# Performance work log

Measured on AMD Instinct MI355X. Metric: run time of the kernel, lower is better.

The kernel has to match this reference:

```python
import jax, jax.numpy as jnp
import numpy as np

N = 100000   # nodes
E = 1600000  # edges
G = 64       # graphs in batch
D = 128      # input_dim
H = 128      # hidden dim (both layers)
C = 10       # output classes
EPS = 1e-5


def setup_inputs() -> dict:
    key = jax.random.key(0)
    ks = jax.random.split(key, 8)
    x = jax.random.normal(ks[0], (N, D), dtype=jnp.float32)
    edge_index = jax.random.randint(ks[1], (2, E), 0, N, dtype=jnp.int32)
    batch = jnp.sort(jax.random.randint(ks[2], (N,), 0, G, dtype=jnp.int32))
    s1 = 1.0 / np.sqrt(D)
    s2 = 1.0 / np.sqrt(H)
    return {
        "x": x, "edge_index": edge_index, "batch": batch,
        "W1": jax.random.uniform(ks[3], (D, H), jnp.float32, -s1, s1),
        "b1": jnp.zeros((H,), jnp.float32),
        "gw1": jnp.ones((H,), jnp.float32),   # GraphNorm weight
        "gb1": jnp.zeros((H,), jnp.float32),  # GraphNorm bias
        "ga1": jnp.ones((H,), jnp.float32),   # GraphNorm mean_scale
        "W2": jax.random.uniform(ks[4], (H, H), jnp.float32, -s2, s2),
        "b2": jnp.zeros((H,), jnp.float32),
        "gw2": jnp.ones((H,), jnp.float32),
        "gb2": jnp.zeros((H,), jnp.float32),
        "ga2": jnp.ones((H,), jnp.float32),
        "Wc": jax.random.uniform(ks[5], (H, C), jnp.float32, -s2, s2),
        "bc": jnp.zeros((C,), jnp.float32),
    }


def _gcn_conv(x, W, b, row, col, deg_inv_sqrt):
    # PyG GCNConv: h = D^-1/2 (A+I) D^-1/2 (x W) + b  (self-loops already in row/col)
    h = x @ W                                   # [N, H]
    norm = deg_inv_sqrt[row] * deg_inv_sqrt[col]  # [E+N]
    msgs = h[row] * norm[:, None]               # gather + scale  [E+N, H]
    out = jax.ops.segment_sum(msgs, col, num_segments=N)  # scatter-add
    return out + b


def _graph_norm(x, batch, counts, weight, bias, mean_scale):
    # PyG GraphNorm: (x - alpha*mean_g) / sqrt(var_g + eps) * weight + bias
    mean = jax.ops.segment_sum(x, batch, num_segments=G) / counts  # [G, H]
    sub = x - mean_scale * mean[batch]
    var = jax.ops.segment_sum(sub * sub, batch, num_segments=G) / counts
    return weight * sub / jnp.sqrt(var[batch] + EPS) + bias


def reference(x, edge_index, batch, W1, b1, gw1, gb1, ga1,
              W2, b2, gw2, gb2, ga2, Wc, bc):
    loops = jnp.arange(N, dtype=edge_index.dtype)
    row = jnp.concatenate([edge_index[0], loops])  # source
    col = jnp.concatenate([edge_index[1], loops])  # target
    deg = jax.ops.segment_sum(jnp.ones_like(col, dtype=x.dtype), col, num_segments=N)
    dis = jnp.where(deg > 0, jax.lax.rsqrt(deg), 0.0)
    counts = jnp.maximum(
        jax.ops.segment_sum(jnp.ones((N,), x.dtype), batch, num_segments=G), 1.0
    )[:, None]  # nodes per graph [G, 1]

    h = jax.nn.relu(_gcn_conv(x, W1, b1, row, col, dis))
    h = _graph_norm(h, batch, counts, gw1, gb1, ga1)
    h = jax.nn.relu(_gcn_conv(h, W2, b2, row, col, dis))
    h = _graph_norm(h, batch, counts, gw2, gb2, ga2)
    # global_mean_pool over graphs, classifier, softmax
    pooled = jax.ops.segment_sum(h, batch, num_segments=G) / counts  # [G, H]
    logits = pooled @ Wc + bc
    return jax.nn.softmax(logits, axis=1)
```

## Files before the change

### kernel.cpp

```cpp
#include <hip/hip_runtime.h>
#include <cstdint>

#define NN 100000
#define NE 1600000
#define NG 64
#define NH 128
#define NC 10
#define EPSV 1e-5f

#define NB 782
#define NBLK 512
#define EPB ((NE + NBLK - 1) / NBLK)
#define NSCAN (NB * NBLK)
#define NSB (NSCAN / 1024)

typedef __attribute__((ext_vector_type(8))) short bf16x8;
typedef __attribute__((ext_vector_type(4))) float f32x4;
typedef __attribute__((ext_vector_type(2))) float f32x2;
typedef unsigned long long u64;
typedef unsigned char uchar;

__device__ __forceinline__ ushort f2b(float f) {
  uint u = __builtin_bit_cast(uint, f);
  u = (u + 0x7FFFu + ((u >> 16) & 1u)) >> 16;
  return (ushort)u;
}
__device__ __forceinline__ float b2f(ushort h) {
  return __builtin_bit_cast(float, ((uint)h) << 16);
}

__global__ __launch_bounds__(256) void k_prep0(const int* __restrict__ batch,
                                               int* __restrict__ gstart, int* __restrict__ counts,
                                               u64* __restrict__ zrowA, u64* __restrict__ zrowB,
                                               const float* __restrict__ W1, ushort* __restrict__ WF1,
                                               const float* __restrict__ W2, ushort* __restrict__ WF2,
                                               const int* __restrict__ ei, int* __restrict__ ghist) {
  int b = blockIdx.x;
  if (b == 0) {
    __shared__ int lb[NG + 1];
    int t = threadIdx.x;
    if (t <= NG) {
      int lo = 0, hi = NN;
      while (lo < hi) { int mid = (lo + hi) >> 1; if (batch[mid] < t) lo = mid + 1; else hi = mid; }
      lb[t] = lo;
    }
    if (t >= 96 && t < 112) zrowA[t - 96] = 0ull;
    if (t >= 112 && t < 128) zrowB[t - 112] = 0ull;
    __syncthreads();
    if (t < NG) { gstart[t] = lb[t]; counts[t] = lb[t + 1] - lb[t]; }
    if (t == 0) gstart[NG] = NN;
  } else if (b <= 16) {
    int tt = (b - 1) * 256 + threadIdx.x;
    const float* W = (tt < 2048) ? W1 : W2;
    ushort* WF = (tt < 2048) ? WF1 : WF2;
    int t = tt & 2047;
    int lane = t & 63, nk = t >> 6;
    int n = nk >> 2, ks = nk & 3;
    int col = n * 16 + (lane & 15);
    int k0 = ks * 32 + (lane >> 4) * 8;
#pragma unroll
    for (int j = 0; j < 8; ++j) WF[(size_t)t * 8 + j] = f2b(W[(k0 + j) * NH + col]);
  } else {
    __shared__ int h[NB];
    int t = threadIdx.x, blk = b - 17;
    for (int i = t; i < NB; i += 256) h[i] = 0;
    __syncthreads();
    int e0 = blk * EPB, e1 = min(NE, e0 + EPB);
    for (int e = e0 + t; e < e1; e += 256) atomicAdd(&h[ei[NE + e] >> 7], 1);
    __syncthreads();
    for (int i = t; i < NB; i += 256) ghist[i * NBLK + blk] = h[i];
  }
}

__global__ __launch_bounds__(256) void k_scan1g(int* __restrict__ data, int* __restrict__ bsums) {
  __shared__ int sh[256];
  int t = threadIdx.x;
  int base = blockIdx.x * 1024 + t * 4;
  int4 v = *reinterpret_cast<const int4*>(data + base);
  int s = v.x + v.y + v.z + v.w;
  sh[t] = s;
  __syncthreads();
  for (int o = 1; o < 256; o <<= 1) {
    int x = (t >= o) ? sh[t - o] : 0;
    __syncthreads();
    sh[t] += x;
    __syncthreads();
  }
  int ex = sh[t] - s;
  int4 o4;
  o4.x = ex; o4.y = ex + v.x; o4.z = ex + v.x + v.y; o4.w = ex + v.x + v.y + v.z;
  *reinterpret_cast<int4*>(data + base) = o4;
  if (t == 255) bsums[blockIdx.x] = sh[255];
}

__global__ __launch_bounds__(512) void k_scan2(int* bsums, int nb) {
  __shared__ int sh[512];
  int t = threadIdx.x;
  int v = (t < nb) ? bsums[t] : 0;
  sh[t] = v;
  __syncthreads();
  for (int o = 1; o < 512; o <<= 1) {
    int x = (t >= o) ? sh[t - o] : 0;
    __syncthreads();
    sh[t] += x;
    __syncthreads();
  }
  if (t < nb) bsums[t] = sh[t] - v;
}

__global__ __launch_bounds__(256) void k_scan3g(int* __restrict__ data, const int* __restrict__ bsums) {
  int t = threadIdx.x;
  int base = blockIdx.x * 1024 + t * 4;
  int add = bsums[blockIdx.x];
  int4 v = *reinterpret_cast<int4*>(data + base);
  v.x += add; v.y += add; v.z += add; v.w += add;
  *reinterpret_cast<int4*>(data + base) = v;
}

__global__ __launch_bounds__(256) void k_scatter(const int* __restrict__ ei, const int* __restrict__ ghist,
                                                 int* __restrict__ tmp) {
  __shared__ int cur[NB];
  int t = threadIdx.x, blk = blockIdx.x;
  for (int i = t; i < NB; i += 256) cur[i] = ghist[i * NBLK + blk];
  __syncthreads();
  int e0 = blk * EPB, e1 = min(NE, e0 + EPB);
  for (int e = e0 + t; e < e1; e += 256) {
    int d = ei[NE + e], s = ei[e];
    int p = atomicAdd(&cur[d >> 7], 1);
    tmp[p] = ((d & 127) << 17) | s;
  }
}

__global__ __launch_bounds__(256) void k_fine(const int* __restrict__ tmp, const int* __restrict__ ghist,
                                              int* __restrict__ deg, int* __restrict__ offs,
                                              float* __restrict__ dis, int* __restrict__ csr) {
  __shared__ int fh[128], fsc[128], fc[128];
  int b = blockIdx.x, t = threadIdx.x;
  int bs = ghist[b * NBLK];
  int be = (b + 1 < NB) ? ghist[(b + 1) * NBLK] : NE;
  if (t < 128) fh[t] = 0;
  __syncthreads();
  for (int e = bs + t; e < be; e += 256) atomicAdd(&fh[tmp[e] >> 17], 1);
  __syncthreads();
  if (t < 128) fsc[t] = fh[t];
  __syncthreads();
  for (int o = 1; o < 128; o <<= 1) {
    int x = 0;
    if (t < 128 && t >= o) x = fsc[t - o];
    __syncthreads();
    if (t < 128) fsc[t] += x;
    __syncthreads();
  }
  if (t < 128) {
    int ex = fsc[t] - fh[t];
    int node = b * 128 + t;
    fc[t] = bs + ex;
    if (node < NN) {
      deg[node] = fh[t];
      offs[node] = bs + ex;
      dis[node] = rsqrtf((float)(fh[t] + 1));
    }
  }
  __syncthreads();
  for (int e = bs + t; e < be; e += 256) {
    int v = tmp[e];
    int p = atomicAdd(&fc[v >> 17], 1);
    csr[p] = v & 0x1FFFF;
  }
}

template <bool NORM>
__global__ __launch_bounds__(256) void k_gemm(const void* __restrict__ Xv, const ushort* __restrict__ WF,
                                              const float* __restrict__ dis, const int* __restrict__ batch,
                                              const float* __restrict__ Aaff, const float* __restrict__ Baff,
                                              uchar* __restrict__ out) {
  __shared__ uint sds[4][512];
  int t = threadIdx.x;
  int w = t >> 6, lane = t & 63;
  int r0 = blockIdx.x * 64 + w * 16;
  int arow = r0 + (lane & 15);
  int khi = lane >> 4;
  int arowc = (arow < NN) ? arow : (NN - 1);

  f32x4 acc[8];
#pragma unroll
  for (int n = 0; n < 8; ++n) acc[n] = (f32x4){0.f, 0.f, 0.f, 0.f};

  int g = 0;
  if (NORM) g = batch[arowc];
  const bf16x8* WFv = reinterpret_cast<const bf16x8*>(WF);

#pragma unroll
  for (int ks = 0; ks < 4; ++ks) {
    int k0 = ks * 32 + khi * 8;
    bf16x8 a;
    if (!NORM) {
      const float* X = (const float*)Xv;
      float4 x0 = *reinterpret_cast<const float4*>(X + (size_t)arowc * NH + k0);
      float4 x1 = *reinterpret_cast<const float4*>(X + (size_t)arowc * NH + k0 + 4);
      a[0] = (short)f2b(x0.x); a[1] = (short)f2b(x0.y); a[2] = (short)f2b(x0.z); a[3] = (short)f2b(x0.w);
      a[4] = (short)f2b(x1.x); a[5] = (short)f2b(x1.y); a[6] = (short)f2b(x1.z); a[7] = (short)f2b(x1.w);
    } else {
      const uchar* X8 = (const uchar*)Xv;
      u64 v = *reinterpret_cast<const u64*>(X8 + (size_t)arowc * NH + k0);
      uint lo = (uint)v, hi = (uint)(v >> 32);
      f32x2 x01 = __builtin_amdgcn_cvt_pk_f32_fp8((int)lo, false);
      f32x2 x23 = __builtin_amdgcn_cvt_pk_f32_fp8((int)lo, true);
      f32x2 x45 = __builtin_amdgcn_cvt_pk_f32_fp8((int)hi, false);
      f32x2 x67 = __builtin_amdgcn_cvt_pk_f32_fp8((int)hi, true);
      float4 A0 = *reinterpret_cast<const float4*>(Aaff + g * NH + k0);
      float4 A1 = *reinterpret_cast<const float4*>(Aaff + g * NH + k0 + 4);
      float4 B0 = *reinterpret_cast<const float4*>(Baff + g * NH + k0);
      float4 B1 = *reinterpret_cast<const float4*>(Baff + g * NH + k0 + 4);
      a[0] = (short)f2b(fmaf(A0.x, x01[0], B0.x));
      a[1] = (short)f2b(fmaf(A0.y, x01[1], B0.y));
      a[2] = (short)f2b(fmaf(A0.z, x23[0], B0.z));
      a[3] = (short)f2b(fmaf(A0.w, x23[1], B0.w));
      a[4] = (short)f2b(fmaf(A1.x, x45[0], B1.x));
      a[5] = (short)f2b(fmaf(A1.y, x45[1], B1.y));
      a[6] = (short)f2b(fmaf(A1.z, x67[0], B1.z));
      a[7] = (short)f2b(fmaf(A1.w, x67[1], B1.w));
    }
#pragma unroll
    for (int n = 0; n < 8; ++n) {
      bf16x8 b = WFv[(n * 4 + ks) * 64 + lane];
      acc[n] = __builtin_amdgcn_mfma_f32_16x16x32_bf16(a, b, acc[n], 0, 0, 0);
    }
  }

  int colb = lane & 15;
  uchar* sb = (uchar*)sds[w];
#pragma unroll
  for (int reg = 0; reg < 4; ++reg) {
    int row = khi * 4 + reg;
    int grow = r0 + row;
    float d = (grow < NN) ? dis[grow] : 0.f;
#pragma unroll
    for (int n = 0; n < 8; n += 2) {
      int p2 = __builtin_amdgcn_cvt_pk_fp8_f32(acc[n][reg] * d, acc[n + 1][reg] * d, 0, false);
      sb[row * 128 + n * 16 + colb] = (uchar)(p2 & 0xFF);
      sb[row * 128 + (n + 1) * 16 + colb] = (uchar)((p2 >> 8) & 0xFF);
    }
  }
  __syncthreads();
  const u64* ss = (const u64*)sds[w];
  u64* gout = (u64*)(out + (size_t)r0 * 128);
#pragma unroll
  for (int it = 0; it < 4; ++it) {
    int idx = it * 64 + lane;
    int row = idx >> 4;
    if (r0 + row < NN) __builtin_nontemporal_store(ss[idx], &gout[idx]);
  }
}

__global__ __launch_bounds__(256) void k_agg(const u64* __restrict__ hf8, const int* __restrict__ offs,
                                             const int* __restrict__ deg, const int* __restrict__ csr,
                                             const float* __restrict__ dis, const float* __restrict__ bias,
                                             u64* __restrict__ outb) {
  int w = threadIdx.x >> 6, lane = threadIdx.x & 63;
  int grp = lane >> 4, sub = lane & 15;
  int node = blockIdx.x * 4 + w;
  if (node >= NN) return;
  f32x2 a01 = (f32x2){0.f, 0.f}, a23 = (f32x2){0.f, 0.f};
  f32x2 a45 = (f32x2){0.f, 0.f}, a67 = (f32x2){0.f, 0.f};
#define ACCUM(V)                                                          \
  {                                                                       \
    uint lo_ = (uint)(V), hi_ = (uint)((V) >> 32);                        \
    a01 += __builtin_amdgcn_cvt_pk_f32_fp8((int)lo_, false);              \
    a23 += __builtin_amdgcn_cvt_pk_f32_fp8((int)lo_, true);               \
    a45 += __builtin_amdgcn_cvt_pk_f32_fp8((int)hi_, false);              \
    a67 += __builtin_amdgcn_cvt_pk_f32_fp8((int)hi_, true);               \
  }
#define BATCH(IBASE)                                                      \
  {                                                                       \
    int p0 = beg + (IBASE) + grp;                                         \
    int c0 = __builtin_nontemporal_load(csr + min(p0, lim));              \
    int c1 = __builtin_nontemporal_load(csr + min(p0 + 4, lim));          \
    int c2 = __builtin_nontemporal_load(csr + min(p0 + 8, lim));          \
    int c3 = __builtin_nontemporal_load(csr + min(p0 + 12, lim));         \
    int s0 = (p0 <= lim) ? c0 : NN;                                       \
    int s1 = (p0 + 4 <= lim) ? c1 : NN;                                   \
    int s2 = (p0 + 8 <= lim) ? c2 : NN;                                   \
    int s3 = (p0 + 12 <= lim) ? c3 : NN;                                  \
    u64 v0 = hf8[(size_t)s0 * 16 + sub];                                  \
    u64 v1 = hf8[(size_t)s1 * 16 + sub];                                  \
    u64 v2 = hf8[(size_t)s2 * 16 + sub];                                  \
    u64 v3 = hf8[(size_t)s3 * 16 + sub];                                  \
    ACCUM(v0); ACCUM(v1); ACCUM(v2); ACCUM(v3);                           \
  }
  int beg = __builtin_nontemporal_load(offs + node);
  int cnt = __builtin_nontemporal_load(deg + node);
  if (grp == 0) {
    u64 v = hf8[(size_t)node * 16 + sub];
    ACCUM(v);
  }
  int lim = beg + cnt - 1;
  BATCH(0);
  if (cnt > 16) {
    BATCH(16);
    for (int i = 32; i < cnt; i += 16) BATCH(i);
  }
#undef BATCH
#undef ACCUM
  float a0 = a01[0], a1 = a01[1], a2 = a23[0], a3 = a23[1];
  float a4 = a45[0], a5 = a45[1], a6 = a67[0], a7 = a67[1];
  a0 += __shfl_xor(a0, 16); a0 += __shfl_xor(a0, 32);
  a1 += __shfl_xor(a1, 16); a1 += __shfl_xor(a1, 32);
  a2 += __shfl_xor(a2, 16); a2 += __shfl_xor(a2, 32);
  a3 += __shfl_xor(a3, 16); a3 += __shfl_xor(a3, 32);
  a4 += __shfl_xor(a4, 16); a4 += __shfl_xor(a4, 32);
  a5 += __shfl_xor(a5, 16); a5 += __shfl_xor(a5, 32);
  a6 += __shfl_xor(a6, 16); a6 += __shfl_xor(a6, 32);
  a7 += __shfl_xor(a7, 16); a7 += __shfl_xor(a7, 32);
  if (grp == 0) {
    float d = dis[node];
    float4 bA = *reinterpret_cast<const float4*>(bias + sub * 8);
    float4 bB = *reinterpret_cast<const float4*>(bias + sub * 8 + 4);
    float o0 = fmaxf(fmaf(d, a0, bA.x), 0.f);
    float o1 = fmaxf(fmaf(d, a1, bA.y), 0.f);
    float o2 = fmaxf(fmaf(d, a2, bA.z), 0.f);
    float o3 = fmaxf(fmaf(d, a3, bA.w), 0.f);
    float o4 = fmaxf(fmaf(d, a4, bB.x), 0.f);
    float o5 = fmaxf(fmaf(d, a5, bB.y), 0.f);
    float o6 = fmaxf(fmaf(d, a6, bB.z), 0.f);
    float o7 = fmaxf(fmaf(d, a7, bB.w), 0.f);
    uint b01 = (uint)__builtin_amdgcn_cvt_pk_fp8_f32(o0, o1, 0, false) & 0xFFFFu;
    uint b23 = (uint)__builtin_amdgcn_cvt_pk_fp8_f32(o2, o3, 0, false) & 0xFFFFu;
    uint b45 = (uint)__builtin_amdgcn_cvt_pk_fp8_f32(o4, o5, 0, false) & 0xFFFFu;
    uint b67 = (uint)__builtin_amdgcn_cvt_pk_fp8_f32(o6, o7, 0, false) & 0xFFFFu;
    u64 pk = (u64)(b01 | (b23 << 16)) | ((u64)(b45 | (b67 << 16)) << 32);
    __builtin_nontemporal_store(pk, &outb[(size_t)node * 16 + sub]);
  }
}

__global__ __launch_bounds__(256) void k_stats(const uint* __restrict__ t8, const int* __restrict__ gstart,
                                               float* __restrict__ acc) {
  int g = blockIdx.x >> 4, s = blockIdx.x & 15;
  int beg = gstart[g], end = gstart[g + 1];
  int j = threadIdx.x & 31, q = threadIdx.x >> 5;
  f32x2 s01 = (f32x2){0.f, 0.f}, s23 = (f32x2){0.f, 0.f};
  f32x2 q01 = (f32x2){0.f, 0.f}, q23 = (f32x2){0.f, 0.f};
  for (int n = beg + s * 8 + q; n < end; n += 128) {
    uint v = t8[(size_t)n * 32 + j];
    f32x2 f01 = __builtin_amdgcn_cvt_pk_f32_fp8((int)v, false);
    f32x2 f23 = __builtin_amdgcn_cvt_pk_f32_fp8((int)v, true);
    s01 += f01; s23 += f23;
    q01 += f01 * f01; q23 += f23 * f23;
  }
  __shared__ float shs[256][4];
  __shared__ float shq[256][4];
  int t = threadIdx.x;
  shs[t][0] = s01[0]; shs[t][1] = s01[1]; shs[t][2] = s23[0]; shs[t][3] = s23[1];
  shq[t][0] = q01[0]; shq[t][1] = q01[1]; shq[t][2] = q23[0]; shq[t][3] = q23[1];
  __syncthreads();
  if (q == 0) {
    float sm[4], sq[4];
#pragma unroll
    for (int k = 0; k < 4; ++k) { sm[k] = shs[j][k]; sq[k] = shq[j][k]; }
#pragma unroll
    for (int qq = 1; qq < 8; ++qq) {
      int idx = qq * 32 + j;
#pragma unroll
      for (int k = 0; k < 4; ++k) { sm[k] += shs[idx][k]; sq[k] += shq[idx][k]; }
    }
    int f = j * 4;
    float* dst = acc + (size_t)(s * NG + g) * 2 * NH;
#pragma unroll
    for (int k = 0; k < 4; ++k) { dst[f + k] = sm[k]; dst[NH + f + k] = sq[k]; }
  }
}

__global__ __launch_bounds__(128) void k_fin1(const float* __restrict__ acc, const int* __restrict__ counts,
                                              const float* __restrict__ gw, const float* __restrict__ gb,
                                              const float* __restrict__ ga,
                                              float* __restrict__ Aaff, float* __restrict__ Baff) {
  int g = blockIdx.x, f = threadIdx.x;
  float sum = 0.f, sq = 0.f;
#pragma unroll 4
  for (int s = 0; s < 16; ++s) {
    const float* d = acc + (size_t)(s * NG + g) * 2 * NH;
    sum += d[f];
    sq += d[NH + f];
  }
  float cnt = fmaxf((float)counts[g], 1.f);
  float m = sum / cnt;
  float ex2 = sq / cnt;
  float a = ga[f];
  float var = ex2 - 2.f * a * m * m + a * a * m * m;
  float rstd = rsqrtf(var + EPSV);
  float A = gw[f] * rstd;
  Aaff[g * NH + f] = A;
  Baff[g * NH + f] = gb[f] - A * a * m;
}

__global__ __launch_bounds__(128) void k_fin2head(const float* __restrict__ acc, const int* __restrict__ counts,
                                                  const float* __restrict__ gw, const float* __restrict__ gb,
                                                  const float* __restrict__ ga, const float* __restrict__ Wc,
                                                  const float* __restrict__ bc, float* __restrict__ outp) {
  __shared__ float pool[NH];
  __shared__ float lg[NC];
  int g = blockIdx.x, f = threadIdx.x;
  float sum = 0.f, sq = 0.f;
#pragma unroll 4
  for (int s = 0; s < 16; ++s) {
    const float* d = acc + (size_t)(s * NG + g) * 2 * NH;
    sum += d[f];
    sq += d[NH + f];
  }
  float cnt = fmaxf((float)counts[g], 1.f);
  float m = sum / cnt;
  float ex2 = sq / cnt;
  float a = ga[f];
  float var = ex2 - 2.f * a * m * m + a * a * m * m;
  float rstd = rsqrtf(var + EPSV);
  pool[f] = gw[f] * rstd * (m - a * m) + gb[f];
  __syncthreads();
  if (f < NC) {
    float s = bc[f];
    for (int h = 0; h < NH; ++h) s = fmaf(pool[h], Wc[h * NC + f], s);
    lg[f] = s;
  }
  __syncthreads();
  if (f == 0) {
    float mx = lg[0];
    for (int c = 1; c < NC; ++c) mx = fmaxf(mx, lg[c]);
    float ex[NC];
    float ssum = 0.f;
    for (int c = 0; c < NC; ++c) { ex[c] = __expf(lg[c] - mx); ssum += ex[c]; }
    float inv = 1.f / ssum;
    for (int c = 0; c < NC; ++c) outp[g * NC + c] = ex[c] * inv;
  }
}

extern "C" void kernel_launch(void* const* d_in, const int* in_sizes, int n_in,
                              void* d_out, int out_size, void* d_ws, size_t ws_size,
                              hipStream_t stream) {
  const float* x   = (const float*)d_in[0];
  const int*   ei  = (const int*)d_in[1];
  const int*   bat = (const int*)d_in[2];
  const float* W1  = (const float*)d_in[3];
  const float* b1  = (const float*)d_in[4];
  const float* gw1 = (const float*)d_in[5];
  const float* gb1 = (const float*)d_in[6];
  const float* ga1 = (const float*)d_in[7];
  const float* W2  = (const float*)d_in[8];
  const float* b2  = (const float*)d_in[9];
  const float* gw2 = (const float*)d_in[10];
  const float* gb2 = (const float*)d_in[11];
  const float* ga2 = (const float*)d_in[12];
  const float* Wc  = (const float*)d_in[13];
  const float* bc  = (const float*)d_in[14];
  float* outp = (float*)d_out;

  char* ws = (char*)d_ws;
  size_t off = 0;
  auto alloc = [&](size_t b) { size_t p = off; off += (b + 255) & ~(size_t)255; return p; };
  int*    deg     = (int*)(ws + alloc((size_t)NN * 4));
  float*  dis     = (float*)(ws + alloc((size_t)NN * 4));
  int*    counts  = (int*)(ws + alloc(NG * 4));
  int*    gstart  = (int*)(ws + alloc((NG + 1) * 4));
  int*    offs    = (int*)(ws + alloc((size_t)NN * 4));
  int*    bsums   = (int*)(ws + alloc(512 * 4));
  int*    csr     = (int*)(ws + alloc((size_t)NE * 4));
  float*  statacc = (float*)(ws + alloc((size_t)16 * NG * 2 * NH * 4));
  float*  Aaff    = (float*)(ws + alloc((size_t)NG * NH * 4));
  float*  Baff    = (float*)(ws + alloc((size_t)NG * NH * 4));
  ushort* WF1     = (ushort*)(ws + alloc((size_t)2048 * 8 * 2));
  ushort* WF2     = (ushort*)(ws + alloc((size_t)2048 * 8 * 2));
  uchar*  bufA    = (uchar*)(ws + alloc((size_t)(NN + 1) * NH));
  uchar*  bufB    = (uchar*)(ws + alloc((size_t)(NN + 1) * NH));
  int* tmp   = (int*)bufB;
  int* ghist = (int*)((char*)bufB + (((size_t)NE * 4 + 255) & ~(size_t)255));
  (void)ws_size; (void)in_sizes; (void)n_in; (void)out_size;

  u64* zrowA = (u64*)(bufA + (size_t)NN * NH);
  u64* zrowB = (u64*)(bufB + (size_t)NN * NH);

  k_prep0<<<529, 256, 0, stream>>>(bat, gstart, counts, zrowA, zrowB, W1, WF1, W2, WF2, ei, ghist);
  k_scan1g<<<NSB, 256, 0, stream>>>(ghist, bsums);
  k_scan2<<<1, 512, 0, stream>>>(bsums, NSB);
  k_scan3g<<<NSB, 256, 0, stream>>>(ghist, bsums);
  k_scatter<<<NBLK, 256, 0, stream>>>(ei, ghist, tmp);
  k_fine<<<NB, 256, 0, stream>>>(tmp, ghist, deg, offs, dis, csr);

  int gemm_grid = (NN + 63) / 64;
  int agg_grid  = (NN + 3) / 4;

  k_gemm<false><<<gemm_grid, 256, 0, stream>>>(x, WF1, dis, bat, nullptr, nullptr, bufA);
  k_agg<<<agg_grid, 256, 0, stream>>>((const u64*)bufA, offs, deg, csr, dis, b1, (u64*)bufB);
  k_stats<<<NG * 16, 256, 0, stream>>>((const uint*)bufB, gstart, statacc);
  k_fin1<<<NG, 128, 0, stream>>>(statacc, counts, gw1, gb1, ga1, Aaff, Baff);

  k_gemm<true><<<gemm_grid, 256, 0, stream>>>(bufB, WF2, dis, bat, Aaff, Baff, bufA);
  k_agg<<<agg_grid, 256, 0, stream>>>((const u64*)bufA, offs, deg, csr, dis, b2, (u64*)bufB);
  k_stats<<<NG * 16, 256, 0, stream>>>((const uint*)bufB, gstart, statacc);
  k_fin2head<<<NG, 128, 0, stream>>>(statacc, counts, gw2, gb2, ga2, Wc, bc, outp);
}
```

Measured before the change: 221.9 us.

## Map one 16-lane group per node in aggregation and fold scan fixup into consumers

The aggregation kernel now assigns each 16-lane group its own destination node instead of having four groups share one node. Each group walks its full neighbour list in batches of 16 loads, which removes the cross-group shuffle reduction and lets all four groups write output. Separately, the scan add-back kernel is dropped, and the scatter and fine-binning kernels add the block prefix sums on the fly. The aggregation change raises register use for 16 outstanding loads per lane, and it can cause divergence when nodes in one wave have different degrees. It also relies on NN being divisible by 16, since the bounds check was removed.

```diff
diff --git a/kernel.cpp b/kernel.cpp
--- a/kernel.cpp
+++ b/kernel.cpp
@@ -108,20 +108,14 @@
   if (t < nb) bsums[t] = sh[t] - v;
 }
 
-__global__ __launch_bounds__(256) void k_scan3g(int* __restrict__ data, const int* __restrict__ bsums) {
-  int t = threadIdx.x;
-  int base = blockIdx.x * 1024 + t * 4;
-  int add = bsums[blockIdx.x];
-  int4 v = *reinterpret_cast<int4*>(data + base);
-  v.x += add; v.y += add; v.z += add; v.w += add;
-  *reinterpret_cast<int4*>(data + base) = v;
-}
-
 __global__ __launch_bounds__(256) void k_scatter(const int* __restrict__ ei, const int* __restrict__ ghist,
-                                                 int* __restrict__ tmp) {
+                                                 const int* __restrict__ bsums, int* __restrict__ tmp) {
   __shared__ int cur[NB];
   int t = threadIdx.x, blk = blockIdx.x;
-  for (int i = t; i < NB; i += 256) cur[i] = ghist[i * NBLK + blk];
+  for (int i = t; i < NB; i += 256) {
+    int idx = i * NBLK + blk;
+    cur[i] = ghist[idx] + bsums[idx >> 10];
+  }
   __syncthreads();
   int e0 = blk * EPB, e1 = min(NE, e0 + EPB);
   for (int e = e0 + t; e < e1; e += 256) {
@@ -132,12 +126,18 @@
 }
 
 __global__ __launch_bounds__(256) void k_fine(const int* __restrict__ tmp, const int* __restrict__ ghist,
+                                              const int* __restrict__ bsums,
                                               int* __restrict__ deg, int* __restrict__ offs,
                                               float* __restrict__ dis, int* __restrict__ csr) {
   __shared__ int fh[128], fsc[128], fc[128];
   int b = blockIdx.x, t = threadIdx.x;
-  int bs = ghist[b * NBLK];
-  int be = (b + 1 < NB) ? ghist[(b + 1) * NBLK] : NE;
+  int idx0 = b * NBLK;
+  int bs = ghist[idx0] + bsums[idx0 >> 10];
+  int be = NE;
+  if (b + 1 < NB) {
+    int idx1 = (b + 1) * NBLK;
+    be = ghist[idx1] + bsums[idx1 >> 10];
+  }
   if (t < 128) fh[t] = 0;
   __syncthreads();
   for (int e = bs + t; e < be; e += 256) atomicAdd(&fh[tmp[e] >> 17], 1);
@@ -259,8 +259,7 @@
                                              u64* __restrict__ outb) {
   int w = threadIdx.x >> 6, lane = threadIdx.x & 63;
   int grp = lane >> 4, sub = lane & 15;
-  int node = blockIdx.x * 4 + w;
-  if (node >= NN) return;
+  int node = (blockIdx.x * 4 + w) * 4 + grp;
   f32x2 a01 = (f32x2){0.f, 0.f}, a23 = (f32x2){0.f, 0.f};
   f32x2 a45 = (f32x2){0.f, 0.f}, a67 = (f32x2){0.f, 0.f};
 #define ACCUM(V)                                                          \
@@ -271,66 +270,51 @@
     a45 += __builtin_amdgcn_cvt_pk_f32_fp8((int)hi_, false);              \
     a67 += __builtin_amdgcn_cvt_pk_f32_fp8((int)hi_, true);               \
   }
+  int beg = __builtin_nontemporal_load(offs + node);
+  int cnt = __builtin_nontemporal_load(deg + node);
+  {
+    u64 v = hf8[(size_t)node * 16 + sub];
+    ACCUM(v);
+  }
+  int lim = max(beg + cnt - 1, 0);
+  int endp = beg + cnt;
 #define BATCH(IBASE)                                                      \
   {                                                                       \
-    int p0 = beg + (IBASE) + grp;                                         \
-    int c0 = __builtin_nontemporal_load(csr + min(p0, lim));              \
-    int c1 = __builtin_nontemporal_load(csr + min(p0 + 4, lim));          \
-    int c2 = __builtin_nontemporal_load(csr + min(p0 + 8, lim));          \
-    int c3 = __builtin_nontemporal_load(csr + min(p0 + 12, lim));         \
-    int s0 = (p0 <= lim) ? c0 : NN;                                       \
-    int s1 = (p0 + 4 <= lim) ? c1 : NN;                                   \
-    int s2 = (p0 + 8 <= lim) ? c2 : NN;                                   \
-    int s3 = (p0 + 12 <= lim) ? c3 : NN;                                  \
-    u64 v0 = hf8[(size_t)s0 * 16 + sub];                                  \
-    u64 v1 = hf8[(size_t)s1 * 16 + sub];                                  \
-    u64 v2 = hf8[(size_t)s2 * 16 + sub];                                  \
-    u64 v3 = hf8[(size_t)s3 * 16 + sub];                                  \
-    ACCUM(v0); ACCUM(v1); ACCUM(v2); ACCUM(v3);                           \
-  }
-  int beg = __builtin_nontemporal_load(offs + node);
-  int cnt = __builtin_nontemporal_load(deg + node);
-  if (grp == 0) {
-    u64 v = hf8[(size_t)node * 16 + sub];
-    ACCUM(v);
-  }
-  int lim = beg + cnt - 1;
+    int pb = beg + (IBASE);                                               \
+    int c_[16];                                                           \
+    _Pragma("unroll")                                                     \
+    for (int j = 0; j < 16; ++j)                                          \
+      c_[j] = __builtin_nontemporal_load(csr + min(pb + j, lim));         \
+    u64 v_[16];                                                           \
+    _Pragma("unroll")                                                     \
+    for (int j = 0; j < 16; ++j) {                                        \
+      int s = (pb + j < endp) ? c_[j] : NN;                               \
+      v_[j] = hf8[(size_t)s * 16 + sub];                                  \
+    }                                                                     \
+    _Pragma("unroll")                                                     \
+    for (int j = 0; j < 16; ++j) ACCUM(v_[j]);                            \
+  }
   BATCH(0);
-  if (cnt > 16) {
-    BATCH(16);
-    for (int i = 32; i < cnt; i += 16) BATCH(i);
-  }
+  for (int i = 16; i < cnt; i += 16) BATCH(i);
 #undef BATCH
 #undef ACCUM
-  float a0 = a01[0], a1 = a01[1], a2 = a23[0], a3 = a23[1];
-  float a4 = a45[0], a5 = a45[1], a6 = a67[0], a7 = a67[1];
-  a0 += __shfl_xor(a0, 16); a0 += __shfl_xor(a0, 32);
-  a1 += __shfl_xor(a1, 16); a1 += __shfl_xor(a1, 32);
-  a2 += __shfl_xor(a2, 16); a2 += __shfl_xor(a2, 32);
-  a3 += __shfl_xor(a3, 16); a3 += __shfl_xor(a3, 32);
-  a4 += __shfl_xor(a4, 16); a4 += __shfl_xor(a4, 32);
-  a5 += __shfl_xor(a5, 16); a5 += __shfl_xor(a5, 32);
-  a6 += __shfl_xor(a6, 16); a6 += __shfl_xor(a6, 32);
-  a7 += __shfl_xor(a7, 16); a7 += __shfl_xor(a7, 32);
-  if (grp == 0) {
-    float d = dis[node];
-    float4 bA = *reinterpret_cast<const float4*>(bias + sub * 8);
-    float4 bB = *reinterpret_cast<const float4*>(bias + sub * 8 + 4);
-    float o0 = fmaxf(fmaf(d, a0, bA.x), 0.f);
-    float o1 = fmaxf(fmaf(d, a1, bA.y), 0.f);
-    float o2 = fmaxf(fmaf(d, a2, bA.z), 0.f);
-    float o3 = fmaxf(fmaf(d, a3, bA.w), 0.f);
-    float o4 = fmaxf(fmaf(d, a4, bB.x), 0.f);
-    float o5 = fmaxf(fmaf(d, a5, bB.y), 0.f);
-    float o6 = fmaxf(fmaf(d, a6, bB.z), 0.f);
-    float o7 = fmaxf(fmaf(d, a7, bB.w), 0.f);
-    uint b01 = (uint)__builtin_amdgcn_cvt_pk_fp8_f32(o0, o1, 0, false) & 0xFFFFu;
-    uint b23 = (uint)__builtin_amdgcn_cvt_pk_fp8_f32(o2, o3, 0, false) & 0xFFFFu;
-    uint b45 = (uint)__builtin_amdgcn_cvt_pk_fp8_f32(o4, o5, 0, false) & 0xFFFFu;
-    uint b67 = (uint)__builtin_amdgcn_cvt_pk_fp8_f32(o6, o7, 0, false) & 0xFFFFu;
-    u64 pk = (u64)(b01 | (b23 << 16)) | ((u64)(b45 | (b67 << 16)) << 32);
-    __builtin_nontemporal_store(pk, &outb[(size_t)node * 16 + sub]);
-  }
+  float d = dis[node];
+  float4 bA = *reinterpret_cast<const float4*>(bias + sub * 8);
+  float4 bB = *reinterpret_cast<const float4*>(bias + sub * 8 + 4);
+  float o0 = fmaxf(fmaf(d, a01[0], bA.x), 0.f);
+  float o1 = fmaxf(fmaf(d, a01[1], bA.y), 0.f);
+  float o2 = fmaxf(fmaf(d, a23[0], bA.z), 0.f);
+  float o3 = fmaxf(fmaf(d, a23[1], bA.w), 0.f);
+  float o4 = fmaxf(fmaf(d, a45[0], bB.x), 0.f);
+  float o5 = fmaxf(fmaf(d, a45[1], bB.y), 0.f);
+  float o6 = fmaxf(fmaf(d, a67[0], bB.z), 0.f);
+  float o7 = fmaxf(fmaf(d, a67[1], bB.w), 0.f);
+  uint b01 = (uint)__builtin_amdgcn_cvt_pk_fp8_f32(o0, o1, 0, false) & 0xFFFFu;
+  uint b23 = (uint)__builtin_amdgcn_cvt_pk_fp8_f32(o2, o3, 0, false) & 0xFFFFu;
+  uint b45 = (uint)__builtin_amdgcn_cvt_pk_fp8_f32(o4, o5, 0, false) & 0xFFFFu;
+  uint b67 = (uint)__builtin_amdgcn_cvt_pk_fp8_f32(o6, o7, 0, false) & 0xFFFFu;
+  u64 pk = (u64)(b01 | (b23 << 16)) | ((u64)(b45 | (b67 << 16)) << 32);
+  __builtin_nontemporal_store(pk, &outb[(size_t)node * 16 + sub]);
 }
 
 __global__ __launch_bounds__(256) void k_stats(const uint* __restrict__ t8, const int* __restrict__ gstart,
@@ -479,12 +463,11 @@
   k_prep0<<<529, 256, 0, stream>>>(bat, gstart, counts, zrowA, zrowB, W1, WF1, W2, WF2, ei, ghist);
   k_scan1g<<<NSB, 256, 0, stream>>>(ghist, bsums);
   k_scan2<<<1, 512, 0, stream>>>(bsums, NSB);
-  k_scan3g<<<NSB, 256, 0, stream>>>(ghist, bsums);
-  k_scatter<<<NBLK, 256, 0, stream>>>(ei, ghist, tmp);
-  k_fine<<<NB, 256, 0, stream>>>(tmp, ghist, deg, offs, dis, csr);
+  k_scatter<<<NBLK, 256, 0, stream>>>(ei, ghist, bsums, tmp);
+  k_fine<<<NB, 256, 0, stream>>>(tmp, ghist, bsums, deg, offs, dis, csr);
 
   int gemm_grid = (NN + 63) / 64;
-  int agg_grid  = (NN + 3) / 4;
+  int agg_grid  = NN / 16;
 
   k_gemm<false><<<gemm_grid, 256, 0, stream>>>(x, WF1, dis, bat, nullptr, nullptr, bufA);
   k_agg<<<agg_grid, 256, 0, stream>>>((const u64*)bufA, offs, deg, csr, dis, b1, (u64*)bufB);
```

Measured after the change: 200.5 us. 9.6% less time.
